# Performance work log

Measured on AMD Instinct MI355X. Metric: run time of the kernel, lower is better.

Reference implementation:

```python
import jax, jax.numpy as jnp
import numpy as np

L, D, H, F_IN = 3, 256, 8, 5
HD = D // H
FF = 4 * D
EPS = 1e-5


def _layer_norm(x, g, b):
    mu = jnp.mean(x, axis=-1, keepdims=True)
    var = jnp.mean(jnp.square(x - mu), axis=-1, keepdims=True)
    return (x - mu) * jax.lax.rsqrt(var + EPS) * g + b


def setup_inputs() -> dict:
    key = jax.random.key(0)
    ks = jax.random.split(key, 20)
    s = 0.02
    inp = {
        'x': jax.random.normal(ks[0], (32, 512, F_IN), jnp.float32),
        'mask': jax.random.randint(ks[1], (32, 512), 0, 2) == 1,
        'Win': jax.random.normal(ks[2], (F_IN, D), jnp.float32) * s,
        'bin_': jnp.zeros((D,), jnp.float32),
        'Wq': jax.random.normal(ks[3], (L, D, D), jnp.float32) * s,
        'bq': jnp.zeros((L, D), jnp.float32),
        'Wk': jax.random.normal(ks[4], (L, D, D), jnp.float32) * s,
        'bk': jnp.zeros((L, D), jnp.float32),
        'Wv': jax.random.normal(ks[5], (L, D, D), jnp.float32) * s,
        'bv': jnp.zeros((L, D), jnp.float32),
        'Wo': jax.random.normal(ks[6], (L, D, D), jnp.float32) * s,
        'bo': jnp.zeros((L, D), jnp.float32),
        'g1': jnp.ones((L, D), jnp.float32),
        'b1': jnp.zeros((L, D), jnp.float32),
        'W1': jax.random.normal(ks[7], (L, D, FF), jnp.float32) * s,
        'c1': jnp.zeros((L, FF), jnp.float32),
        'W2': jax.random.normal(ks[8], (L, FF, D), jnp.float32) * s,
        'c2': jnp.zeros((L, D), jnp.float32),
        'g2': jnp.ones((L, D), jnp.float32),
        'b2': jnp.zeros((L, D), jnp.float32),
    }
    return inp


def reference(x, mask, Win, bin_, Wq, bq, Wk, bk, Wv, bv, Wo, bo, g1, b1, W1, c1, W2, c2, g2, b2):
    B, S, _ = x.shape
    scale = 1.0 / jnp.sqrt(jnp.float32(HD))
    h = x @ Win + bin_  # [B,S,D]
    kmask = mask[:, None, None, :]  # [B,1,1,S] key-padding mask
    for l in range(L):
        q = (h @ Wq[l] + bq[l]).reshape(B, S, H, HD).transpose(0, 2, 1, 3)
        k = (h @ Wk[l] + bk[l]).reshape(B, S, H, HD).transpose(0, 2, 1, 3)
        v = (h @ Wv[l] + bv[l]).reshape(B, S, H, HD).transpose(0, 2, 1, 3)
        scores = jnp.einsum('bhqd,bhkd->bhqk', q, k) * scale
        scores = jnp.where(kmask, -jnp.inf, scores)
        attn = jnp.nan_to_num(jax.nn.softmax(scores, axis=-1), nan=0.0)
        ao = jnp.einsum('bhqk,bhkd->bhqd', attn, v).transpose(0, 2, 1, 3).reshape(B, S, D)
        ao = ao @ Wo[l] + bo[l]
        h = _layer_norm(h + ao, g1[l], b1[l])
        ff = jax.nn.relu(h @ W1[l] + c1[l]) @ W2[l] + c2[l]
        h = _layer_norm(h + ff, g2[l], b2[l])
    return h
```

## Files before the change

kernel.cpp:

```cpp
#include <hip/hip_runtime.h>
#include <cstdint>

#define NLAYER 3
#define DMODEL 256
#define NHEAD 8
#define HEADD 32
#define FFDIM 1024
#define BATCH 32
#define SEQ 512
#define MTOK (BATCH*SEQ)

typedef __attribute__((ext_vector_type(8))) __bf16 bf16x8;
typedef __attribute__((ext_vector_type(4))) __bf16 bf16x4;
typedef __attribute__((ext_vector_type(4))) float f32x4;
typedef __attribute__((ext_vector_type(16))) float f32x16;

typedef __attribute__((address_space(1))) const uint8_t ga_t;
typedef __attribute__((address_space(3))) uint8_t la_t;
__device__ __forceinline__ void gll16(const void* g, void* l) {
    __builtin_amdgcn_global_load_lds((ga_t*)g, (la_t*)l, 16, 0, 0);
}

__global__ __launch_bounds__(256)
void prep_kernel(const float* __restrict__ Wq, const float* __restrict__ Wk,
                 const float* __restrict__ Wv, const float* __restrict__ Wo,
                 const float* __restrict__ W1, const float* __restrict__ W2,
                 const float* __restrict__ bq, const float* __restrict__ bk,
                 const float* __restrict__ bv,
                 __bf16* __restrict__ wqkv, __bf16* __restrict__ wot,
                 __bf16* __restrict__ w1t, __bf16* __restrict__ w2t,
                 float* __restrict__ bqkv,
                 const float* __restrict__ x, const float* __restrict__ Win,
                 const float* __restrict__ bin, __bf16* __restrict__ h16)
{
    const int bid = blockIdx.x;
    const int tid = threadIdx.x;
    if (bid >= 2313) {
        const int m0 = (bid - 2313) * 8;
        const float bv_ = bin[tid];
#pragma unroll
        for (int p = 0; p < 8; ++p) {
            const int m = m0 + p;
            const float* xr = x + (size_t)m * 5;
            float acc = bv_;
#pragma unroll
            for (int k = 0; k < 5; ++k) acc += xr[k] * Win[k * DMODEL + tid];
            h16[(size_t)m * DMODEL + tid] = (__bf16)acc;
        }
        return;
    }
    if (bid >= 3 * 768) {
        int idx = (bid - 3 * 768) * 256 + tid;
        int l = idx / 768, j = idx % 768;
        float v = (j < 256) ? bq[l * 256 + j]
                : (j < 512) ? bk[l * 256 + j - 256]
                            : bv[l * 256 + j - 512];
        bqkv[idx] = v;
        return;
    }
    const int l = bid / 768;
    const int rr = bid % 768;
    const float* src; __bf16* dst; int K, N, t;
    if (rr < 192) {
        int ty = rr >> 6; t = rr & 63;
        src = (ty == 0 ? Wq : ty == 1 ? Wk : Wv) + (size_t)l * 65536;
        dst = wqkv + (size_t)l * 768 * 256 + (size_t)ty * 65536;
        K = 256; N = 256;
    } else if (rr < 256) {
        t = rr - 192; src = Wo + (size_t)l * 65536; dst = wot + (size_t)l * 65536;
        K = 256; N = 256;
    } else if (rr < 512) {
        t = rr - 256; src = W1 + (size_t)l * 262144; dst = w1t + (size_t)l * 262144;
        K = 256; N = 1024;
    } else {
        t = rr - 512; src = W2 + (size_t)l * 262144; dst = w2t + (size_t)l * 262144;
        K = 1024; N = 256;
    }
    const int tn = N >> 5;
    const int tk = t / tn, tj = t % tn;
    __shared__ float tile[32][33];
    const int c = tid & 31, rbase = tid >> 5;
#pragma unroll
    for (int p = 0; p < 4; ++p) {
        int kr = rbase + p * 8;
        tile[kr][c] = src[(size_t)(tk * 32 + kr) * N + tj * 32 + c];
    }
    __syncthreads();
#pragma unroll
    for (int p = 0; p < 4; ++p) {
        int nr = rbase + p * 8;
        dst[(size_t)(tj * 32 + nr) * K + tk * 32 + c] = (__bf16)tile[c][nr];
    }
}

template<int RELU>
__global__ __launch_bounds__(256, 3)
void gemm_kernel(const __bf16* __restrict__ A, const __bf16* __restrict__ Bt,
                 const float* __restrict__ bias,
                 __bf16* __restrict__ C, int M, int N, int K)
{
    __shared__ __bf16 As[128 * 64];
    __shared__ __bf16 Bs[128 * 64];
    const int tid = threadIdx.x;
    const int m0 = blockIdx.x * 128;
    const int n0 = blockIdx.y * 128;
    const int lane = tid & 63;
    const int wave = tid >> 6;
    const int wm = (wave & 1) * 64;
    const int wn = (wave >> 1) * 64;
    const int fr = lane & 15;
    const int quad = lane >> 4;
    const int lr = lane >> 3;
    const int qg = (lane & 7) ^ lr;

    const __bf16* Ab = A  + (size_t)(m0 + wave * 32 + lr) * K + qg * 8;
    const __bf16* Bb = Bt + (size_t)(n0 + wave * 32 + lr) * K + qg * 8;

    f32x4 acc[4][4];
#pragma unroll
    for (int i = 0; i < 4; ++i)
#pragma unroll
        for (int j = 0; j < 4; ++j)
#pragma unroll
            for (int r = 0; r < 4; ++r) acc[i][j][r] = 0.f;

    const int frs = fr & 7;

    for (int k0 = 0; k0 < K; k0 += 64) {
#pragma unroll
        for (int j = 0; j < 4; ++j) {
            gll16(Ab + (size_t)j * 8 * K + k0, As + (wave * 4 + j) * 512);
            gll16(Bb + (size_t)j * 8 * K + k0, Bs + (wave * 4 + j) * 512);
        }
        __syncthreads();
#pragma unroll
        for (int kk = 0; kk < 2; ++kk) {
            bf16x8 af[4], bfr[4];
#pragma unroll
            for (int i = 0; i < 4; ++i) {
                int row = wm + i * 16 + fr;
                af[i] = *(const bf16x8*)(As + row * 64 + (((kk * 4 + quad) ^ frs) * 8));
            }
#pragma unroll
            for (int j = 0; j < 4; ++j) {
                int row = wn + j * 16 + fr;
                bfr[j] = *(const bf16x8*)(Bs + row * 64 + (((kk * 4 + quad) ^ frs) * 8));
            }
#pragma unroll
            for (int i = 0; i < 4; ++i)
#pragma unroll
                for (int j = 0; j < 4; ++j)
                    acc[i][j] = __builtin_amdgcn_mfma_f32_16x16x32_bf16(
                        af[i], bfr[j], acc[i][j], 0, 0, 0);
        }
        __syncthreads();
    }

#pragma unroll
    for (int i = 0; i < 4; ++i) {
#pragma unroll
        for (int j = 0; j < 4; ++j) {
            const int gc = n0 + wn + j * 16 + fr;
            const float bv = bias[gc];
#pragma unroll
            for (int r = 0; r < 4; ++r) {
                const int gr = m0 + wm + i * 16 + quad * 4 + r;
                float v = acc[i][j][r] + bv;
                if (RELU) v = fmaxf(v, 0.f);
                C[(size_t)gr * N + gc] = (__bf16)v;
            }
        }
    }
}

template<int LAST>
__global__ __launch_bounds__(256, 4)
void gemm_ln_kernel(const __bf16* __restrict__ A, const __bf16* __restrict__ Bt,
                    const float* __restrict__ bias, const __bf16* __restrict__ res,
                    const float* __restrict__ g, const float* __restrict__ be,
                    __bf16* __restrict__ out16, float* __restrict__ out32, int K)
{
    __shared__ __bf16 As[32 * 64];
    __shared__ __bf16 Bs[256 * 64];
    __shared__ float red[32 * 8];
    const int tid = threadIdx.x;
    const int m0 = blockIdx.x * 32;
    const int lane = tid & 63;
    const int wave = tid >> 6;
    const int wn = wave * 64;
    const int fr = lane & 15;
    const int quad = lane >> 4;
    const int lr = lane >> 3;
    const int qg = (lane & 7) ^ lr;
    const int frs = fr & 7;

    const __bf16* Ab = A  + (size_t)(m0 + wave * 8 + lr) * K + qg * 8;
    const __bf16* Bb = Bt + (size_t)(wave * 64 + lr) * K + qg * 8;

    f32x4 acc[2][4];
#pragma unroll
    for (int i = 0; i < 2; ++i)
#pragma unroll
        for (int j = 0; j < 4; ++j)
#pragma unroll
            for (int r = 0; r < 4; ++r) acc[i][j][r] = 0.f;

    for (int k0 = 0; k0 < K; k0 += 64) {
        gll16(Ab + k0, As + wave * 512);
#pragma unroll
        for (int p = 0; p < 8; ++p)
            gll16(Bb + (size_t)p * 8 * K + k0, Bs + (wave * 8 + p) * 512);
        __syncthreads();
#pragma unroll
        for (int kk = 0; kk < 2; ++kk) {
            bf16x8 af[2], bfr[4];
#pragma unroll
            for (int i = 0; i < 2; ++i) {
                int row = i * 16 + fr;
                af[i] = *(const bf16x8*)(As + row * 64 + (((kk * 4 + quad) ^ frs) * 8));
            }
#pragma unroll
            for (int j = 0; j < 4; ++j) {
                int row = wn + j * 16 + fr;
                bfr[j] = *(const bf16x8*)(Bs + row * 64 + (((kk * 4 + quad) ^ frs) * 8));
            }
#pragma unroll
            for (int i = 0; i < 2; ++i)
#pragma unroll
                for (int j = 0; j < 4; ++j)
                    acc[i][j] = __builtin_amdgcn_mfma_f32_16x16x32_bf16(
                        af[i], bfr[j], acc[i][j], 0, 0, 0);
        }
        __syncthreads();
    }

    float bv[4];
#pragma unroll
    for (int j = 0; j < 4; ++j) bv[j] = bias[wn + j * 16 + fr];

#pragma unroll
    for (int i = 0; i < 2; ++i) {
#pragma unroll
        for (int r = 0; r < 4; ++r) {
            const int row = i * 16 + quad * 4 + r;
            float ps = 0.f, pq = 0.f;
#pragma unroll
            for (int j = 0; j < 4; ++j) {
                const int gc = wn + j * 16 + fr;
                float v = acc[i][j][r] + bv[j]
                        + (float)res[(size_t)(m0 + row) * DMODEL + gc];
                acc[i][j][r] = v;
                ps += v;
                pq += v * v;
            }
#pragma unroll
            for (int off = 1; off < 16; off <<= 1) {
                ps += __shfl_xor(ps, off, 64);
                pq += __shfl_xor(pq, off, 64);
            }
            if (fr == 0) {
                red[row * 8 + wave * 2]     = ps;
                red[row * 8 + wave * 2 + 1] = pq;
            }
        }
    }
    __syncthreads();

#pragma unroll
    for (int i = 0; i < 2; ++i) {
#pragma unroll
        for (int r = 0; r < 4; ++r) {
            const int row = i * 16 + quad * 4 + r;
            f32x4 a = *(const f32x4*)(red + row * 8);
            f32x4 b2 = *(const f32x4*)(red + row * 8 + 4);
            const float s  = a[0] + a[2] + b2[0] + b2[2];
            const float sq = a[1] + a[3] + b2[1] + b2[3];
            const float mu = s * (1.f / DMODEL);
            const float var = sq * (1.f / DMODEL) - mu * mu;
            const float rs = rsqrtf(var + 1e-5f);
#pragma unroll
            for (int j = 0; j < 4; ++j) {
                const int gc = wn + j * 16 + fr;
                float y = (acc[i][j][r] - mu) * rs * g[gc] + be[gc];
                if (LAST) out32[(size_t)(m0 + row) * DMODEL + gc] = y;
                else      out16[(size_t)(m0 + row) * DMODEL + gc] = (__bf16)y;
            }
        }
    }
}

__global__ __launch_bounds__(1024)
void attn_kernel(const __bf16* __restrict__ qkv, const int* __restrict__ mask,
                 __bf16* __restrict__ ao)
{
    __shared__ __bf16 Ks[512 * 40];
    __shared__ __bf16 Vt[32 * 520];
    __shared__ __bf16 Pq[16 * 32 * 40];
    __shared__ float maskadd[512];

    const int b = blockIdx.x >> 3;
    const int h = blockIdx.x & 7;
    const int t = threadIdx.x;
    const int lane = t & 63;
    const int wave = t >> 6;
    const int cl = lane & 31;
    const int kh = lane >> 5;
    const float scale = 0.17677669529663687f;

    const size_t base = (size_t)b * SEQ * 768;

#pragma unroll
    for (int p = 0; p < 2; ++p) {
        int idx = p * 1024 + t;
        int key = idx >> 2, ch = idx & 3;
        bf16x8 kv = *(const bf16x8*)(qkv + base + (size_t)key * 768 + 256 + h * 32 + ch * 8);
        *(bf16x8*)(Ks + key * 40 + ch * 8) = kv;
        bf16x8 vv = *(const bf16x8*)(qkv + base + (size_t)key * 768 + 512 + h * 32 + ch * 8);
#pragma unroll
        for (int j = 0; j < 8; ++j) Vt[(ch * 8 + j) * 520 + key] = vv[j];
    }
    if (t < 512) maskadd[t] = mask[b * SEQ + t] ? -1e30f : 0.f;
    __syncthreads();

    const int q0 = wave * 32;
    const __bf16* qrow = qkv + base + (size_t)(q0 + cl) * 768 + h * 32;
    bf16x8 qf0 = *(const bf16x8*)(qrow + kh * 8);
    bf16x8 qf1 = *(const bf16x8*)(qrow + 16 + kh * 8);

    f32x16 oacc;
#pragma unroll
    for (int i = 0; i < 16; ++i) oacc[i] = 0.f;
    float lsum = 0.f;
    __bf16* Pw = Pq + wave * 32 * 40;

    for (int kt = 0; kt < SEQ; kt += 32) {
        bf16x8 kf0 = *(const bf16x8*)(Ks + (kt + cl) * 40 + kh * 8);
        bf16x8 kf1 = *(const bf16x8*)(Ks + (kt + cl) * 40 + 16 + kh * 8);
        f32x16 s;
#pragma unroll
        for (int i = 0; i < 16; ++i) s[i] = 0.f;
        s = __builtin_amdgcn_mfma_f32_32x32x16_bf16(kf0, qf0, s, 0, 0, 0);
        s = __builtin_amdgcn_mfma_f32_32x32x16_bf16(kf1, qf1, s, 0, 0, 0);
        float pv[16];
#pragma unroll
        for (int g = 0; g < 4; ++g) {
            f32x4 mv = *(const f32x4*)(maskadd + kt + 8 * g + 4 * kh);
#pragma unroll
            for (int r = 0; r < 4; ++r) {
                float e = __expf(s[g * 4 + r] * scale + mv[r]);
                pv[g * 4 + r] = e;
                lsum += e;
            }
        }
#pragma unroll
        for (int g = 0; g < 4; ++g) {
            bf16x4 pb;
#pragma unroll
            for (int r = 0; r < 4; ++r) pb[r] = (__bf16)pv[g * 4 + r];
            *(bf16x4*)(Pw + cl * 40 + 8 * g + 4 * kh) = pb;
        }
        bf16x8 pf0 = *(const bf16x8*)(Pw + cl * 40 + kh * 8);
        bf16x8 pf1 = *(const bf16x8*)(Pw + cl * 40 + 16 + kh * 8);
        bf16x8 vf0 = *(const bf16x8*)(Vt + cl * 520 + kt + kh * 8);
        bf16x8 vf1 = *(const bf16x8*)(Vt + cl * 520 + kt + 16 + kh * 8);
        oacc = __builtin_amdgcn_mfma_f32_32x32x16_bf16(vf0, pf0, oacc, 0, 0, 0);
        oacc = __builtin_amdgcn_mfma_f32_32x32x16_bf16(vf1, pf1, oacc, 0, 0, 0);
    }

    lsum += __shfl_xor(lsum, 32);
    const float inv = (lsum > 0.f) ? 1.f / lsum : 0.f;
    __bf16* orow = ao + (size_t)(b * SEQ + q0 + cl) * DMODEL + h * 32;
#pragma unroll
    for (int g = 0; g < 4; ++g) {
        bf16x4 w;
#pragma unroll
        for (int r = 0; r < 4; ++r) w[r] = (__bf16)(oacc[g * 4 + r] * inv);
        *(bf16x4*)(orow + 8 * g + 4 * kh) = w;
    }
}

extern "C" void kernel_launch(void* const* d_in, const int* in_sizes, int n_in,
                              void* d_out, int out_size, void* d_ws, size_t ws_size,
                              hipStream_t stream)
{
    const float* x   = (const float*)d_in[0];
    const int*   mask= (const int*)d_in[1];
    const float* Win = (const float*)d_in[2];
    const float* bin = (const float*)d_in[3];
    const float* Wq  = (const float*)d_in[4];
    const float* bq  = (const float*)d_in[5];
    const float* Wk  = (const float*)d_in[6];
    const float* bk  = (const float*)d_in[7];
    const float* Wv  = (const float*)d_in[8];
    const float* bv  = (const float*)d_in[9];
    const float* Wo  = (const float*)d_in[10];
    const float* bo  = (const float*)d_in[11];
    const float* g1  = (const float*)d_in[12];
    const float* b1  = (const float*)d_in[13];
    const float* W1  = (const float*)d_in[14];
    const float* c1  = (const float*)d_in[15];
    const float* W2  = (const float*)d_in[16];
    const float* c2  = (const float*)d_in[17];
    const float* g2  = (const float*)d_in[18];
    const float* b2  = (const float*)d_in[19];

    char* ws = (char*)d_ws;
    size_t off = 0;
    auto alloc = [&](size_t bytes) -> void* {
        void* p = ws + off;
        off += (bytes + 255) & ~(size_t)255;
        return p;
    };
    __bf16* hA   = (__bf16*)alloc((size_t)MTOK * 256 * 2);
    __bf16* hB   = (__bf16*)alloc((size_t)MTOK * 256 * 2);
    __bf16* u    = (__bf16*)alloc((size_t)MTOK * 1024 * 2);
    __bf16* qkv  = u;
    __bf16* ffT  = u;
    __bf16* ao   = (__bf16*)alloc((size_t)MTOK * 256 * 2);
    __bf16* wqkv = (__bf16*)alloc((size_t)3 * 768 * 256 * 2);
    __bf16* wot  = (__bf16*)alloc((size_t)3 * 256 * 256 * 2);
    __bf16* w1t  = (__bf16*)alloc((size_t)3 * 1024 * 256 * 2);
    __bf16* w2t  = (__bf16*)alloc((size_t)3 * 256 * 1024 * 2);
    float*  bqkv = (float*)alloc((size_t)3 * 768 * 4);

    prep_kernel<<<dim3(2313 + MTOK / 8), dim3(256), 0, stream>>>(
        Wq, Wk, Wv, Wo, W1, W2, bq, bk, bv, wqkv, wot, w1t, w2t, bqkv,
        x, Win, bin, hA);

    for (int l = 0; l < NLAYER; ++l) {
        gemm_kernel<0><<<dim3(128, 6), dim3(256), 0, stream>>>(
            hA, wqkv + (size_t)l * 768 * 256, bqkv + l * 768, qkv, MTOK, 768, 256);
        attn_kernel<<<dim3(256), dim3(1024), 0, stream>>>(qkv, mask, ao);
        gemm_ln_kernel<0><<<dim3(MTOK / 32), dim3(256), 0, stream>>>(
            ao, wot + (size_t)l * 65536, bo + l * 256, hA,
            g1 + l * 256, b1 + l * 256, hB, nullptr, 256);
        gemm_kernel<1><<<dim3(128, 8), dim3(256), 0, stream>>>(
            hB, w1t + (size_t)l * 262144, c1 + l * 1024, ffT, MTOK, 1024, 256);
        if (l == 2) {
            gemm_ln_kernel<1><<<dim3(MTOK / 32), dim3(256), 0, stream>>>(
                ffT, w2t + (size_t)l * 262144, c2 + l * 256, hB,
                g2 + l * 256, b2 + l * 256, nullptr, (float*)d_out, 1024);
        } else {
            gemm_ln_kernel<0><<<dim3(MTOK / 32), dim3(256), 0, stream>>>(
                ffT, w2t + (size_t)l * 262144, c2 + l * 256, hB,
                g2 + l * 256, b2 + l * 256, hA, nullptr, 1024);
        }
    }
}
```

Baseline: 366.9 us.

## Keep full weight tile resident in LDS and double-buffer A slices in GEMM

The projection/FFN-up GEMM now loads the whole 128x256 weight tile into LDS once, with a rotated layout to avoid bank conflicts. It then streams the activation tile in 32-wide K slices through a double buffer, so loads of the next slice overlap MFMA work and only one barrier is needed per step. K is hardcoded to 256 and the occupancy hint drops to two blocks per CU because LDS use grows to about 80KB. This risks lower occupancy and a longer initial load before compute starts.

```diff
diff --git a/kernel.cpp b/kernel.cpp
--- a/kernel.cpp
+++ b/kernel.cpp
@@ -94,13 +94,13 @@
 }
 
 template<int RELU>
-__global__ __launch_bounds__(256, 3)
+__global__ __launch_bounds__(256, 2)
 void gemm_kernel(const __bf16* __restrict__ A, const __bf16* __restrict__ Bt,
                  const float* __restrict__ bias,
-                 __bf16* __restrict__ C, int M, int N, int K)
+                 __bf16* __restrict__ C, int N)
 {
-    __shared__ __bf16 As[128 * 64];
-    __shared__ __bf16 Bs[128 * 64];
+    __shared__ __bf16 Bs[128 * 256];
+    __shared__ __bf16 As[2][64 * 64];
     const int tid = threadIdx.x;
     const int m0 = blockIdx.x * 128;
     const int n0 = blockIdx.y * 128;
@@ -110,11 +110,33 @@
     const int wn = (wave >> 1) * 64;
     const int fr = lane & 15;
     const int quad = lane >> 4;
-    const int lr = lane >> 3;
-    const int qg = (lane & 7) ^ lr;
-
-    const __bf16* Ab = A  + (size_t)(m0 + wave * 32 + lr) * K + qg * 8;
-    const __bf16* Bb = Bt + (size_t)(n0 + wave * 32 + lr) * K + qg * 8;
+
+    {
+        const int rsub = lane >> 5;
+#pragma unroll
+        for (int c = 0; c < 16; ++c) {
+            const int rl = wave * 32 + c * 2 + rsub;
+            const int g = ((lane & 31) - 4 * rl) & 31;
+            gll16(Bt + (size_t)(n0 + rl) * 256 + g * 8,
+                  Bs + (wave * 32 + c * 2) * 256);
+        }
+    }
+    const int arow8 = lane >> 3;
+    const int apos = lane & 7;
+#define STAGE_A(ks, buf)                                                      \
+    {                                                                         \
+        _Pragma("unroll")                                                     \
+        for (int s_ = 0; s_ < 2; ++s_) {                                      \
+            const int c_ = wave * 2 + s_;                                     \
+            const int row_ = c_ * 8 + arow8;                                  \
+            const int g_ = apos ^ (row_ & 7);                                 \
+            gll16(A + (size_t)(m0 + row_ + 64 * (g_ >> 2)) * 256              \
+                    + (ks) * 32 + (g_ & 3) * 8,                               \
+                  &As[buf][c_ * 8 * 64]);                                     \
+        }                                                                     \
+    }
+    STAGE_A(0, 0);
+    __syncthreads();
 
     f32x4 acc[4][4];
 #pragma unroll
@@ -124,37 +146,33 @@
 #pragma unroll
             for (int r = 0; r < 4; ++r) acc[i][j][r] = 0.f;
 
-    const int frs = fr & 7;
-
-    for (int k0 = 0; k0 < K; k0 += 64) {
+    const int aposr = ((wave & 1) * 4 + quad) ^ (fr & 7);
+
+#pragma unroll
+    for (int ks = 0; ks < 8; ++ks) {
+        if (ks < 7) STAGE_A(ks + 1, (ks + 1) & 1);
+        const __bf16* Ab = As[ks & 1];
+        bf16x8 af[4], bfr[4];
+#pragma unroll
+        for (int i = 0; i < 4; ++i) {
+            const int row = i * 16 + fr;
+            af[i] = *(const bf16x8*)(Ab + row * 64 + aposr * 8);
+        }
 #pragma unroll
         for (int j = 0; j < 4; ++j) {
-            gll16(Ab + (size_t)j * 8 * K + k0, As + (wave * 4 + j) * 512);
-            gll16(Bb + (size_t)j * 8 * K + k0, Bs + (wave * 4 + j) * 512);
-        }
+            const int row = wn + j * 16 + fr;
+            const int pos = (ks * 4 + quad + 4 * fr) & 31;
+            bfr[j] = *(const bf16x8*)(Bs + row * 256 + pos * 8);
+        }
+#pragma unroll
+        for (int i = 0; i < 4; ++i)
+#pragma unroll
+            for (int j = 0; j < 4; ++j)
+                acc[i][j] = __builtin_amdgcn_mfma_f32_16x16x32_bf16(
+                    af[i], bfr[j], acc[i][j], 0, 0, 0);
         __syncthreads();
-#pragma unroll
-        for (int kk = 0; kk < 2; ++kk) {
-            bf16x8 af[4], bfr[4];
-#pragma unroll
-            for (int i = 0; i < 4; ++i) {
-                int row = wm + i * 16 + fr;
-                af[i] = *(const bf16x8*)(As + row * 64 + (((kk * 4 + quad) ^ frs) * 8));
-            }
-#pragma unroll
-            for (int j = 0; j < 4; ++j) {
-                int row = wn + j * 16 + fr;
-                bfr[j] = *(const bf16x8*)(Bs + row * 64 + (((kk * 4 + quad) ^ frs) * 8));
-            }
-#pragma unroll
-            for (int i = 0; i < 4; ++i)
-#pragma unroll
-                for (int j = 0; j < 4; ++j)
-                    acc[i][j] = __builtin_amdgcn_mfma_f32_16x16x32_bf16(
-                        af[i], bfr[j], acc[i][j], 0, 0, 0);
-        }
-        __syncthreads();
-    }
+    }
+#undef STAGE_A
 
 #pragma unroll
     for (int i = 0; i < 4; ++i) {
@@ -429,13 +447,13 @@
 
     for (int l = 0; l < NLAYER; ++l) {
         gemm_kernel<0><<<dim3(128, 6), dim3(256), 0, stream>>>(
-            hA, wqkv + (size_t)l * 768 * 256, bqkv + l * 768, qkv, MTOK, 768, 256);
+            hA, wqkv + (size_t)l * 768 * 256, bqkv + l * 768, qkv, 768);
         attn_kernel<<<dim3(256), dim3(1024), 0, stream>>>(qkv, mask, ao);
         gemm_ln_kernel<0><<<dim3(MTOK / 32), dim3(256), 0, stream>>>(
             ao, wot + (size_t)l * 65536, bo + l * 256, hA,
             g1 + l * 256, b1 + l * 256, hB, nullptr, 256);
         gemm_kernel<1><<<dim3(128, 8), dim3(256), 0, stream>>>(
-            hB, w1t + (size_t)l * 262144, c1 + l * 1024, ffT, MTOK, 1024, 256);
+            hB, w1t + (size_t)l * 262144, c1 + l * 1024, ffT, 1024);
         if (l == 2) {
             gemm_ln_kernel<1><<<dim3(MTOK / 32), dim3(256), 0, stream>>>(
                 ffT, w2t + (size_t)l * 262144, c2 + l * 256, hB,
```

Measured after the change: 367.7 us. About the same (+0.2%).
